# Performance work log

Hardware: AMD Instinct MI355X
Metric: run time of the kernel (lower is better)

Reference implementation:

```python
import jax, jax.numpy as jnp
import numpy as np

B, S, D, H, E, FF = 8, 512, 768, 12, 8, 3072
HD = D // H

def layernorm(x, g, b, eps=1e-5):
    mu = jnp.mean(x, axis=-1, keepdims=True)
    var = jnp.mean((x - mu) ** 2, axis=-1, keepdims=True)
    return (x - mu) * jax.lax.rsqrt(var + eps) * g + b

def setup_inputs() -> dict:
    key = jax.random.key(0)
    ks = jax.random.split(key, 16)
    sd = lambda n: 1.0 / np.sqrt(n)
    return {
        "x": jax.random.normal(ks[0], (B, S, D), jnp.float32),
        "indexes_list": jax.random.randint(ks[1], (1,), 0, E),
        "ln1_g": jnp.ones((D,), jnp.float32),
        "ln1_b": jnp.zeros((D,), jnp.float32),
        "qkv_w": jax.random.normal(ks[2], (D, 3 * D), jnp.float32) * sd(D),
        "proj_w": jax.random.normal(ks[3], (D, D), jnp.float32) * sd(D),
        "proj_b": jnp.zeros((D,), jnp.float32),
        "ln2_g": jnp.ones((D,), jnp.float32),
        "ln2_b": jnp.zeros((D,), jnp.float32),
        "switch_w": jax.random.normal(ks[4], (D, E), jnp.float32) * sd(D),
        "switch_b": jnp.zeros((E,), jnp.float32),
        "w1": jax.random.normal(ks[5], (E, D, FF), jnp.float32) * sd(D),
        "b1": jnp.zeros((E, FF), jnp.float32),
        "w2": jax.random.normal(ks[6], (E, FF, D), jnp.float32) * sd(FF),
        "b2": jnp.zeros((E, D), jnp.float32),
    }

def reference(x, indexes_list, ln1_g, ln1_b, qkv_w, proj_w, proj_b,
              ln2_g, ln2_b, switch_w, switch_b, w1, b1, w2, b2):
    # --- attention sublayer ---
    h = layernorm(x, ln1_g, ln1_b)
    qkv = (h @ qkv_w).reshape(B, S, 3, H, HD).transpose(2, 0, 3, 1, 4)  # [3,B,H,S,hd]
    q, k, v = qkv[0], qkv[1], qkv[2]
    scale = HD ** -0.5
    attn = jax.nn.softmax(jnp.einsum('bhqd,bhkd->bhqk', q, k) * scale, axis=-1)
    o = jnp.einsum('bhqk,bhkd->bhqd', attn, v).transpose(0, 2, 1, 3).reshape(B, S, D)
    x = x + o @ proj_w + proj_b
    # --- switch MoE sublayer (routes arg ignored, as in original) ---
    h = layernorm(x, ln2_g, ln2_b).reshape(B * S, D)  # [T,D]
    logits = h @ switch_w + switch_b
    routes = jnp.argmax(jax.nn.softmax(logits, axis=-1), axis=-1)  # [T]
    # dense per-expert compute, then select by route (same math as gather/scatter)
    y = jax.nn.gelu(jnp.einsum('td,edf->etf', h, w1) + b1[:, None, :], approximate=False)
    y = jax.nn.gelu(jnp.einsum('etf,efd->etd', y, w2) + b2[:, None, :], approximate=False)
    moe_out = y[routes, jnp.arange(B * S)]  # [T,D]
    return x + moe_out.reshape(B, S, D)
```

## Files before the change

kernel.cpp:

```cpp
#include <hip/hip_runtime.h>
#include <math.h>

#define T_TOK   4096
#define D_MODEL 768
#define H_HEADS 12
#define HDIM    64
#define S_SEQ   512
#define B_BATCH 8
#define E_EXP   8
#define FF_DIM  3072
#define MAX_TILES 40
#define MPAD_MAX  (MAX_TILES * 128)
#define KSPLIT  4

typedef __attribute__((ext_vector_type(8))) short short8;
typedef __attribute__((ext_vector_type(4))) float floatx4;

__device__ __forceinline__ float gelu_exact(float x) {
    return 0.5f * x * (1.0f + erff(x * 0.7071067811865476f));
}

__device__ __forceinline__ unsigned short f2bf(float f) {
    unsigned int u = __float_as_uint(f);
    u += 0x7fffu + ((u >> 16) & 1u);
    return (unsigned short)(u >> 16);
}
__device__ __forceinline__ float bf2f(unsigned short h) {
    return __uint_as_float(((unsigned int)h) << 16);
}
__device__ __forceinline__ void split_bf(float v, unsigned short& hi, unsigned short& lo) {
    hi = f2bf(v);
    lo = f2bf(v - bf2f(hi));
}

__device__ __forceinline__ void gload16(const void* g, void* l) {
    __builtin_amdgcn_global_load_lds(
        (const __attribute__((address_space(1))) unsigned int*)g,
        (__attribute__((address_space(3))) unsigned int*)l, 16, 0, 0);
}
__device__ __forceinline__ int swz3(int r) { return (r ^ (r >> 2)) & 3; }

__global__ void __launch_bounds__(256) ln_f32(const float* __restrict__ x,
                                              const float* __restrict__ g,
                                              const float* __restrict__ b,
                                              float* __restrict__ out) {
    int row = blockIdx.x;
    const float* xr = x + (size_t)row * D_MODEL;
    int tid = threadIdx.x;
    float v0 = xr[tid], v1 = xr[tid + 256], v2 = xr[tid + 512];
    float s = v0 + v1 + v2;
    float q = v0 * v0 + v1 * v1 + v2 * v2;
    for (int off = 32; off; off >>= 1) {
        s += __shfl_down(s, off);
        q += __shfl_down(q, off);
    }
    __shared__ float rs[4], rq[4], stats[2];
    int wid = tid >> 6, lane = tid & 63;
    if (lane == 0) { rs[wid] = s; rq[wid] = q; }
    __syncthreads();
    if (tid == 0) {
        float ts = rs[0] + rs[1] + rs[2] + rs[3];
        float tq = rq[0] + rq[1] + rq[2] + rq[3];
        float mu = ts * (1.0f / 768.0f);
        float var = tq * (1.0f / 768.0f) - mu * mu;
        stats[0] = mu; stats[1] = rsqrtf(var + 1e-5f);
    }
    __syncthreads();
    float mu = stats[0], rstd = stats[1];
    float* orow = out + (size_t)row * D_MODEL;
    orow[tid]       = (v0 - mu) * rstd * g[tid]       + b[tid];
    orow[tid + 256] = (v1 - mu) * rstd * g[tid + 256] + b[tid + 256];
    orow[tid + 512] = (v2 - mu) * rstd * g[tid + 512] + b[tid + 512];
}

__global__ void __launch_bounds__(256) ln_split(const float* __restrict__ x,
                                                const float* __restrict__ g,
                                                const float* __restrict__ b,
                                                unsigned short* __restrict__ ohi,
                                                unsigned short* __restrict__ olo) {
    int row = blockIdx.x;
    const float* xr = x + (size_t)row * D_MODEL;
    int tid = threadIdx.x;
    float v0 = xr[tid], v1 = xr[tid + 256], v2 = xr[tid + 512];
    float s = v0 + v1 + v2;
    float q = v0 * v0 + v1 * v1 + v2 * v2;
    for (int off = 32; off; off >>= 1) {
        s += __shfl_down(s, off);
        q += __shfl_down(q, off);
    }
    __shared__ float rs[4], rq[4], stats[2];
    int wid = tid >> 6, lane = tid & 63;
    if (lane == 0) { rs[wid] = s; rq[wid] = q; }
    __syncthreads();
    if (tid == 0) {
        float ts = rs[0] + rs[1] + rs[2] + rs[3];
        float tq = rq[0] + rq[1] + rq[2] + rq[3];
        float mu = ts * (1.0f / 768.0f);
        float var = tq * (1.0f / 768.0f) - mu * mu;
        stats[0] = mu; stats[1] = rsqrtf(var + 1e-5f);
    }
    __syncthreads();
    float mu = stats[0], rstd = stats[1];
    unsigned short* hr = ohi + (size_t)row * D_MODEL;
    unsigned short* lr = olo + (size_t)row * D_MODEL;
    float r0 = (v0 - mu) * rstd * g[tid]       + b[tid];
    float r1 = (v1 - mu) * rstd * g[tid + 256] + b[tid + 256];
    float r2 = (v2 - mu) * rstd * g[tid + 512] + b[tid + 512];
    unsigned short hi, lo;
    split_bf(r0, hi, lo); hr[tid] = hi;       lr[tid] = lo;
    split_bf(r1, hi, lo); hr[tid + 256] = hi; lr[tid + 256] = lo;
    split_bf(r2, hi, lo); hr[tid + 512] = hi; lr[tid + 512] = lo;
}

__global__ void __launch_bounds__(256) transpose_bf16(const float* __restrict__ in,
                                                      unsigned short* __restrict__ out,
                                                      int R, int C) {
    __shared__ float t[32][33];
    const float* inb = in + (size_t)blockIdx.z * R * C;
    unsigned short* outb = out + (size_t)blockIdx.z * R * C;
    int c0 = blockIdx.x * 32, r0 = blockIdx.y * 32;
    int tx = threadIdx.x & 31, ty = threadIdx.x >> 5;
#pragma unroll
    for (int rr = 0; rr < 32; rr += 8)
        t[ty + rr][tx] = inb[(size_t)(r0 + ty + rr) * C + c0 + tx];
    __syncthreads();
#pragma unroll
    for (int rr = 0; rr < 32; rr += 8)
        outb[(size_t)(c0 + ty + rr) * R + r0 + tx] = f2bf(t[tx][ty + rr]);
}

__global__ void __launch_bounds__(256) transpose_split(const float* __restrict__ in,
                                                       unsigned short* __restrict__ out_hi,
                                                       unsigned short* __restrict__ out_lo,
                                                       int R, int C) {
    __shared__ float t[32][33];
    int c0 = blockIdx.x * 32, r0 = blockIdx.y * 32;
    int tx = threadIdx.x & 31, ty = threadIdx.x >> 5;
#pragma unroll
    for (int rr = 0; rr < 32; rr += 8)
        t[ty + rr][tx] = in[(size_t)(r0 + ty + rr) * C + c0 + tx];
    __syncthreads();
#pragma unroll
    for (int rr = 0; rr < 32; rr += 8) {
        float v = t[tx][ty + rr];
        unsigned short hi, lo;
        split_bf(v, hi, lo);
        size_t idx = (size_t)(c0 + ty + rr) * R + r0 + tx;
        out_hi[idx] = hi;
        out_lo[idx] = lo;
    }
}

__global__ void __launch_bounds__(256) attn_mfma(const float* __restrict__ qkv,
                                                 unsigned short* __restrict__ ohi,
                                                 unsigned short* __restrict__ olo) {
    __shared__ __align__(16) short Kh[64][72], Kl[64][72];
    __shared__ __align__(16) short Vh[64][72], Vl[64][72];

    int qt = blockIdx.x, hh = blockIdx.y, bb = blockIdx.z;
    int tid = threadIdx.x;
    int lane = tid & 63, wv = tid >> 6;
    int lm = lane & 15, q8 = (lane >> 4) * 8, q4 = (lane >> 4) * 4;
    const size_t rstride = 3 * D_MODEL;
    const float* base = qkv + (size_t)bb * S_SEQ * rstride + hh * HDIM;

    short8 qh[2], ql[2];
    {
        const float* qrow = base + (size_t)(qt * 64 + 16 * wv + lm) * rstride;
#pragma unroll
        for (int ks = 0; ks < 2; ks++) {
            float4 v0 = *(const float4*)(qrow + ks * 32 + q8);
            float4 v1 = *(const float4*)(qrow + ks * 32 + q8 + 4);
            unsigned short h_, l_;
            short8 sh, sl;
            split_bf(v0.x * 0.125f, h_, l_); sh[0] = (short)h_; sl[0] = (short)l_;
            split_bf(v0.y * 0.125f, h_, l_); sh[1] = (short)h_; sl[1] = (short)l_;
            split_bf(v0.z * 0.125f, h_, l_); sh[2] = (short)h_; sl[2] = (short)l_;
            split_bf(v0.w * 0.125f, h_, l_); sh[3] = (short)h_; sl[3] = (short)l_;
            split_bf(v1.x * 0.125f, h_, l_); sh[4] = (short)h_; sl[4] = (short)l_;
            split_bf(v1.y * 0.125f, h_, l_); sh[5] = (short)h_; sl[5] = (short)l_;
            split_bf(v1.z * 0.125f, h_, l_); sh[6] = (short)h_; sl[6] = (short)l_;
            split_bf(v1.w * 0.125f, h_, l_); sh[7] = (short)h_; sl[7] = (short)l_;
            qh[ks] = sh; ql[ks] = sl;
        }
    }

    float m_run[4], l_run[4];
    floatx4 o_acc[4];
#pragma unroll
    for (int i = 0; i < 4; i++) {
        m_run[i] = -1e30f; l_run[i] = 0.f;
        o_acc[i] = (floatx4){0.f, 0.f, 0.f, 0.f};
    }

    int sr = tid >> 2;
    int sc0 = (tid & 3) * 16;

    for (int kt = 0; kt < 8; kt++) {
        __syncthreads();
        {
            const float* krow = base + (size_t)(kt * 64 + sr) * rstride + D_MODEL;
            const float* vrow = krow + D_MODEL;
#pragma unroll
            for (int c = 0; c < 16; c += 4) {
                float4 kv = *(const float4*)(krow + sc0 + c);
                ushort4 h4, l4; unsigned short h_, l_;
                split_bf(kv.x, h_, l_); h4.x = h_; l4.x = l_;
                split_bf(kv.y, h_, l_); h4.y = h_; l4.y = l_;
                split_bf(kv.z, h_, l_); h4.z = h_; l4.z = l_;
                split_bf(kv.w, h_, l_); h4.w = h_; l4.w = l_;
                *(ushort4*)&Kh[sr][sc0 + c] = h4;
                *(ushort4*)&Kl[sr][sc0 + c] = l4;
                float4 vv = *(const float4*)(vrow + sc0 + c);
                split_bf(vv.x, h_, l_); Vh[sc0 + c + 0][sr] = (short)h_; Vl[sc0 + c + 0][sr] = (short)l_;
                split_bf(vv.y, h_, l_); Vh[sc0 + c + 1][sr] = (short)h_; Vl[sc0 + c + 1][sr] = (short)l_;
                split_bf(vv.z, h_, l_); Vh[sc0 + c + 2][sr] = (short)h_; Vl[sc0 + c + 2][sr] = (short)l_;
                split_bf(vv.w, h_, l_); Vh[sc0 + c + 3][sr] = (short)h_; Vl[sc0 + c + 3][sr] = (short)l_;
            }
        }
        __syncthreads();

        floatx4 s_acc[4];
#pragma unroll
        for (int nt = 0; nt < 4; nt++) s_acc[nt] = (floatx4){0.f, 0.f, 0.f, 0.f};
#pragma unroll
        for (int ks = 0; ks < 2; ks++) {
#pragma unroll
            for (int nt = 0; nt < 4; nt++) {
                short8 bh = *(const short8*)&Kh[nt * 16 + lm][ks * 32 + q8];
                short8 bl = *(const short8*)&Kl[nt * 16 + lm][ks * 32 + q8];
                s_acc[nt] = __builtin_amdgcn_mfma_f32_16x16x32_bf16(qh[ks], bh, s_acc[nt], 0, 0, 0);
                s_acc[nt] = __builtin_amdgcn_mfma_f32_16x16x32_bf16(qh[ks], bl, s_acc[nt], 0, 0, 0);
                s_acc[nt] = __builtin_amdgcn_mfma_f32_16x16x32_bf16(ql[ks], bh, s_acc[nt], 0, 0, 0);
            }
        }

        float alpha_r[4];
#pragma unroll
        for (int reg = 0; reg < 4; reg++) {
            float tm = fmaxf(fmaxf(s_acc[0][reg], s_acc[1][reg]),
                             fmaxf(s_acc[2][reg], s_acc[3][reg]));
            tm = fmaxf(tm, __shfl_xor(tm, 1));
            tm = fmaxf(tm, __shfl_xor(tm, 2));
            tm = fmaxf(tm, __shfl_xor(tm, 4));
            tm = fmaxf(tm, __shfl_xor(tm, 8));
            float mn = fmaxf(m_run[reg], tm);
            alpha_r[reg] = __expf(m_run[reg] - mn);
            m_run[reg] = mn;
            float ts = 0.f;
#pragma unroll
            for (int nt = 0; nt < 4; nt++) {
                float pv = __expf(s_acc[nt][reg] - mn);
                s_acc[nt][reg] = pv;
                ts += pv;
            }
            ts += __shfl_xor(ts, 1);
            ts += __shfl_xor(ts, 2);
            ts += __shfl_xor(ts, 4);
            ts += __shfl_xor(ts, 8);
            l_run[reg] = l_run[reg] * alpha_r[reg] + ts;
        }

        __syncthreads();

#pragma unroll
        for (int nt = 0; nt < 4; nt++)
#pragma unroll
            for (int reg = 0; reg < 4; reg++) {
                unsigned short h_, l_;
                split_bf(s_acc[nt][reg], h_, l_);
                Kh[16 * wv + q4 + reg][nt * 16 + lm] = (short)h_;
                Kl[16 * wv + q4 + reg][nt * 16 + lm] = (short)l_;
            }
#pragma unroll
        for (int nt = 0; nt < 4; nt++)
#pragma unroll
            for (int reg = 0; reg < 4; reg++) o_acc[nt][reg] *= alpha_r[reg];

        __syncthreads();

#pragma unroll
        for (int ks = 0; ks < 2; ks++) {
            short8 ph = *(const short8*)&Kh[16 * wv + lm][ks * 32 + q8];
            short8 pl = *(const short8*)&Kl[16 * wv + lm][ks * 32 + q8];
#pragma unroll
            for (int nt = 0; nt < 4; nt++) {
                short8 vh = *(const short8*)&Vh[nt * 16 + lm][ks * 32 + q8];
                short8 vl = *(const short8*)&Vl[nt * 16 + lm][ks * 32 + q8];
                o_acc[nt] = __builtin_amdgcn_mfma_f32_16x16x32_bf16(ph, vh, o_acc[nt], 0, 0, 0);
                o_acc[nt] = __builtin_amdgcn_mfma_f32_16x16x32_bf16(ph, vl, o_acc[nt], 0, 0, 0);
                o_acc[nt] = __builtin_amdgcn_mfma_f32_16x16x32_bf16(pl, vh, o_acc[nt], 0, 0, 0);
            }
        }
    }

    size_t ob = (size_t)(bb * S_SEQ + qt * 64) * D_MODEL + hh * HDIM;
#pragma unroll
    for (int reg = 0; reg < 4; reg++) {
        float inv = 1.0f / l_run[reg];
#pragma unroll
        for (int nt = 0; nt < 4; nt++) {
            unsigned short h_, l_;
            split_bf(o_acc[nt][reg] * inv, h_, l_);
            size_t idx = ob + (size_t)(16 * wv + q4 + reg) * D_MODEL + nt * 16 + lm;
            ohi[idx] = h_;
            olo[idx] = l_;
        }
    }
}

__global__ void __launch_bounds__(64) router_kernel(const float* __restrict__ h2,
                                                    const float* __restrict__ sw,
                                                    const float* __restrict__ sb,
                                                    int* __restrict__ routes,
                                                    int* __restrict__ counts) {
    int t = blockIdx.x;
    int lane = threadIdx.x;
    const float* hr = h2 + (size_t)t * D_MODEL;
    float acc[8] = {};
    for (int d = lane; d < D_MODEL; d += 64) {
        float hv = hr[d];
        const float* wr = sw + (size_t)d * 8;
#pragma unroll
        for (int e = 0; e < 8; e++) acc[e] += hv * wr[e];
    }
#pragma unroll
    for (int e = 0; e < 8; e++)
        for (int off = 32; off; off >>= 1) acc[e] += __shfl_down(acc[e], off);
    if (lane == 0) {
        int best = 0;
        float bv = acc[0] + sb[0];
#pragma unroll
        for (int e = 1; e < 8; e++) {
            float v = acc[e] + sb[e];
            if (v > bv) { bv = v; best = e; }
        }
        routes[t] = best;
        atomicAdd(&counts[best], 1);
    }
}

__global__ void __launch_bounds__(256) init_kernel(int* counts, int* cursor, int* perm) {
    int idx = blockIdx.x * 256 + threadIdx.x;
    if (idx < MPAD_MAX) perm[idx] = -1;
    if (idx < 8) { counts[idx] = 0; cursor[idx] = 0; }
}

__global__ void __launch_bounds__(256) zero_tmp(float* __restrict__ t) {
    size_t i = ((size_t)blockIdx.x * 256 + threadIdx.x) * 4;
    if (i < (size_t)MPAD_MAX * D_MODEL)
        *(float4*)(t + i) = (float4){0.f, 0.f, 0.f, 0.f};
}

__global__ void moe_plan(const int* __restrict__ counts, int* pad_base,
                         int* tile_e, int* tile_row0, int* ntiles) {
    if (threadIdx.x == 0 && blockIdx.x == 0) {
        int base = 0, nt = 0;
        for (int e = 0; e < E_EXP; e++) {
            pad_base[e] = base;
            int c = counts[e];
            int nte = (c + 127) >> 7;
            for (int j = 0; j < nte; j++) {
                tile_e[nt] = e;
                tile_row0[nt] = base + j * 128;
                nt++;
            }
            base += nte * 128;
        }
        ntiles[0] = nt;
    }
}

__global__ void __launch_bounds__(256) scatter_kernel(const int* __restrict__ routes,
                                                      const int* __restrict__ pad_base,
                                                      int* __restrict__ cursor,
                                                      int* __restrict__ perm) {
    int t = blockIdx.x * 256 + threadIdx.x;
    if (t < T_TOK) {
        int e = routes[t];
        int pos = atomicAdd(&cursor[e], 1);
        perm[pad_base[e] + pos] = t;
    }
}

__global__ void __launch_bounds__(256) gather_bf16(const float* __restrict__ h2,
                                                   const int* __restrict__ perm,
                                                   unsigned short* __restrict__ Ag) {
    int g = blockIdx.x;
    int row = perm[g];
    unsigned short* dst = Ag + (size_t)g * D_MODEL;
    if (row >= 0) {
        const float* src = h2 + (size_t)row * D_MODEL;
        for (int d = threadIdx.x; d < D_MODEL; d += 256) dst[d] = f2bf(src[d]);
    } else {
        for (int d = threadIdx.x; d < D_MODEL; d += 256) dst[d] = 0;
    }
}

template <int MODE>
__global__ void __launch_bounds__(256) sgemm(const unsigned short* __restrict__ Ah_,
                                             const unsigned short* __restrict__ Al_,
                                             const unsigned short* __restrict__ Bh_,
                                             const unsigned short* __restrict__ Bl_,
                                             const float* __restrict__ bias,
                                             const float* __restrict__ resid,
                                             float* __restrict__ Cf,
                                             int N, int K) {
    __shared__ __align__(16) short Ah[2][128][32];
    __shared__ __align__(16) short Al[2][128][32];
    __shared__ __align__(16) short Bh[2][128][32];
    __shared__ __align__(16) short Bl[2][128][32];

    int row0 = blockIdx.y * 128, n0 = blockIdx.x * 128;
    int tid = threadIdx.x;
    int lane = tid & 63, wid = tid >> 6;
    int wr0 = (wid >> 1) * 64, wc0 = (wid & 1) * 64;
    int lm = lane & 15, q8 = (lane >> 4) * 8;

    int rch = lane >> 2, sl = lane & 3;
    int rst = wid * 32 + rch;
    int gsb = (sl ^ swz3(rst)) << 4;

    const unsigned short* Ahb = Ah_ + (size_t)row0 * K;
    const unsigned short* Alb = Al_ + (size_t)row0 * K;
    const unsigned short* Bhb = Bh_ + (size_t)n0 * K;
    const unsigned short* Blb = Bl_ + (size_t)n0 * K;

    const char* gAh = (const char*)(Ahb + (size_t)rst * K) + gsb;
    const char* gAl = (const char*)(Alb + (size_t)rst * K) + gsb;
    const char* gBh = (const char*)(Bhb + (size_t)rst * K) + gsb;
    const char* gBl = (const char*)(Blb + (size_t)rst * K) + gsb;
    size_t r16 = (size_t)16 * K * 2;

    auto stage = [&](int b, int t) {
        size_t kb = (size_t)t * 64;
        gload16(gAh + kb,       &Ah[b][wid * 32][0]);
        gload16(gAh + r16 + kb, &Ah[b][wid * 32 + 16][0]);
        gload16(gAl + kb,       &Al[b][wid * 32][0]);
        gload16(gAl + r16 + kb, &Al[b][wid * 32 + 16][0]);
        gload16(gBh + kb,       &Bh[b][wid * 32][0]);
        gload16(gBh + r16 + kb, &Bh[b][wid * 32 + 16][0]);
        gload16(gBl + kb,       &Bl[b][wid * 32][0]);
        gload16(gBl + r16 + kb, &Bl[b][wid * 32 + 16][0]);
    };

    floatx4 acc[4][4];
#pragma unroll
    for (int i = 0; i < 4; i++)
#pragma unroll
        for (int j = 0; j < 4; j++) acc[i][j] = (floatx4){0.f, 0.f, 0.f, 0.f};

    const int NSTEP = K >> 5;
    stage(0, 0);
    __syncthreads();

    int cur = 0;
    for (int t = 0; t < NSTEP; t++) {
        if (t + 1 < NSTEP) stage(cur ^ 1, t + 1);

        short8 ah[4], al[4], bh[4], bl[4];
#pragma unroll
        for (int i = 0; i < 4; i++) {
            int r = wr0 + i * 16 + lm;
            int bo = (q8 * 2) ^ (swz3(r) << 4);
            ah[i] = *(const short8*)((const char*)&Ah[cur][r][0] + bo);
            al[i] = *(const short8*)((const char*)&Al[cur][r][0] + bo);
        }
#pragma unroll
        for (int j = 0; j < 4; j++) {
            int r = wc0 + j * 16 + lm;
            int bo = (q8 * 2) ^ (swz3(r) << 4);
            bh[j] = *(const short8*)((const char*)&Bh[cur][r][0] + bo);
            bl[j] = *(const short8*)((const char*)&Bl[cur][r][0] + bo);
        }
#pragma unroll
        for (int i = 0; i < 4; i++)
#pragma unroll
            for (int j = 0; j < 4; j++) {
                acc[i][j] = __builtin_amdgcn_mfma_f32_16x16x32_bf16(ah[i], bh[j], acc[i][j], 0, 0, 0);
                acc[i][j] = __builtin_amdgcn_mfma_f32_16x16x32_bf16(ah[i], bl[j], acc[i][j], 0, 0, 0);
                acc[i][j] = __builtin_amdgcn_mfma_f32_16x16x32_bf16(al[i], bh[j], acc[i][j], 0, 0, 0);
            }
        __syncthreads();
        cur ^= 1;
    }

    int q4 = (lane >> 4) * 4;
#pragma unroll
    for (int i = 0; i < 4; i++) {
#pragma unroll
        for (int j = 0; j < 4; j++) {
            int c = n0 + wc0 + j * 16 + lm;
#pragma unroll
            for (int reg = 0; reg < 4; reg++) {
                int rloc = wr0 + i * 16 + q4 + reg;
                size_t idx = (size_t)(row0 + rloc) * N + c;
                float v = acc[i][j][reg];
                if constexpr (MODE == 0) Cf[idx] = v;
                else                     Cf[idx] = resid[idx] + v + bias[c];
            }
        }
    }
}

template <int MODE>
__global__ void __launch_bounds__(256) mgemm(const unsigned short* __restrict__ A,
                                             const unsigned short* __restrict__ Bt,
                                             const float* __restrict__ bias,
                                             const float* __restrict__ resid,
                                             float* __restrict__ Cf,
                                             unsigned short* __restrict__ Cb,
                                             int N, int K,
                                             const int* __restrict__ perm,
                                             const int* __restrict__ tile_e,
                                             const int* __restrict__ tile_row0,
                                             const int* __restrict__ ntiles) {
    __shared__ __align__(16) short As[2][128][64];
    __shared__ __align__(16) short Bs[2][128][64];

    if ((int)blockIdx.y >= ntiles[0]) return;
    int e = tile_e[blockIdx.y];
    int row0 = tile_row0[blockIdx.y];
    Bt += (size_t)e * N * K;
    bias += (size_t)e * N;
    int n0 = blockIdx.x * 128;

    int tid = threadIdx.x;
    int lane = tid & 63, wid = tid >> 6;
    int wr0 = (wid >> 1) * 64, wc0 = (wid & 1) * 64;
    int lm = lane & 15, q8 = (lane >> 4) * 8;

    int rl = lane >> 3, sl = lane & 7;
    int gsb = (sl ^ rl) << 4;

    const unsigned short* Abase = A + (size_t)row0 * K;
    const unsigned short* Bbase = Bt + (size_t)n0 * K;
    const char* gA = (const char*)(Abase + (size_t)(wid * 32 + rl) * K) + gsb;
    const char* gB = (const char*)(Bbase + (size_t)(wid * 32 + rl) * K) + gsb;

    auto stage = [&](int b, int t) {
        size_t kb = (size_t)t * 128;
#pragma unroll
        for (int c = 0; c < 4; c++) {
            gload16(gA + (size_t)c * 16 * K + kb, &As[b][wid * 32 + c * 8][0]);
            gload16(gB + (size_t)c * 16 * K + kb, &Bs[b][wid * 32 + c * 8][0]);
        }
    };

    floatx4 acc[4][4];
#pragma unroll
    for (int i = 0; i < 4; i++)
#pragma unroll
        for (int j = 0; j < 4; j++) acc[i][j] = (floatx4){0.f, 0.f, 0.f, 0.f};

    const int NSTEP = K >> 6;
    stage(0, 0);
    __syncthreads();

    int cur = 0;
    for (int t = 0; t < NSTEP; t++) {
        if (t + 1 < NSTEP) stage(cur ^ 1, t + 1);

#pragma unroll
        for (int ks = 0; ks < 2; ks++) {
            short8 af[4], bfr[4];
#pragma unroll
            for (int i = 0; i < 4; i++) {
                int r = wr0 + i * 16 + lm;
                int bo = (ks * 64 + q8 * 2) ^ ((r & 7) << 4);
                af[i] = *(const short8*)((const char*)&As[cur][r][0] + bo);
            }
#pragma unroll
            for (int j = 0; j < 4; j++) {
                int r = wc0 + j * 16 + lm;
                int bo = (ks * 64 + q8 * 2) ^ ((r & 7) << 4);
                bfr[j] = *(const short8*)((const char*)&Bs[cur][r][0] + bo);
            }
#pragma unroll
            for (int i = 0; i < 4; i++)
#pragma unroll
                for (int j = 0; j < 4; j++)
                    acc[i][j] = __builtin_amdgcn_mfma_f32_16x16x32_bf16(af[i], bfr[j], acc[i][j], 0, 0, 0);
        }
        __syncthreads();
        cur ^= 1;
    }

    int q4 = (lane >> 4) * 4;
#pragma unroll
    for (int i = 0; i < 4; i++) {
#pragma unroll
        for (int j = 0; j < 4; j++) {
            int c = n0 + wc0 + j * 16 + lm;
#pragma unroll
            for (int reg = 0; reg < 4; reg++) {
                int rloc = wr0 + i * 16 + q4 + reg;
                float v = acc[i][j][reg];
                if constexpr (MODE == 2) {
                    Cb[(size_t)(row0 + rloc) * N + c] = f2bf(gelu_exact(v + bias[c]));
                } else {
                    int t = perm[row0 + rloc];
                    if (t >= 0) {
                        size_t idx = (size_t)t * N + c;
                        Cf[idx] = resid[idx] + gelu_exact(v + bias[c]);
                    }
                }
            }
        }
    }
}

__global__ void __launch_bounds__(256) kgemm(const unsigned short* __restrict__ A,
                                             const unsigned short* __restrict__ Bt,
                                             float* __restrict__ tmp,
                                             int N, int K,
                                             const int* __restrict__ tile_e,
                                             const int* __restrict__ tile_row0,
                                             const int* __restrict__ ntiles) {
    __shared__ __align__(16) short As[2][128][64];
    __shared__ __align__(16) short Bs[2][128][64];

    if ((int)blockIdx.y >= ntiles[0]) return;
    int e = tile_e[blockIdx.y];
    int row0 = tile_row0[blockIdx.y];
    Bt += (size_t)e * N * K;
    int n0 = blockIdx.x * 128;
    const int KLEN = K / KSPLIT;
    size_t kbase = (size_t)blockIdx.z * KLEN * 2;

    int tid = threadIdx.x;
    int lane = tid & 63, wid = tid >> 6;
    int wr0 = (wid >> 1) * 64, wc0 = (wid & 1) * 64;
    int lm = lane & 15, q8 = (lane >> 4) * 8;

    int rl = lane >> 3, sl = lane & 7;
    int gsb = (sl ^ rl) << 4;

    const unsigned short* Abase = A + (size_t)row0 * K;
    const unsigned short* Bbase = Bt + (size_t)n0 * K;
    const char* gA = (const char*)(Abase + (size_t)(wid * 32 + rl) * K) + gsb + kbase;
    const char* gB = (const char*)(Bbase + (size_t)(wid * 32 + rl) * K) + gsb + kbase;

    auto stage = [&](int b, int t) {
        size_t kb = (size_t)t * 128;
#pragma unroll
        for (int c = 0; c < 4; c++) {
            gload16(gA + (size_t)c * 16 * K + kb, &As[b][wid * 32 + c * 8][0]);
            gload16(gB + (size_t)c * 16 * K + kb, &Bs[b][wid * 32 + c * 8][0]);
        }
    };

    floatx4 acc[4][4];
#pragma unroll
    for (int i = 0; i < 4; i++)
#pragma unroll
        for (int j = 0; j < 4; j++) acc[i][j] = (floatx4){0.f, 0.f, 0.f, 0.f};

    const int NSTEP = KLEN >> 6;
    stage(0, 0);
    __syncthreads();

    int cur = 0;
    for (int t = 0; t < NSTEP; t++) {
        if (t + 1 < NSTEP) stage(cur ^ 1, t + 1);

#pragma unroll
        for (int ks = 0; ks < 2; ks++) {
            short8 af[4], bfr[4];
#pragma unroll
            for (int i = 0; i < 4; i++) {
                int r = wr0 + i * 16 + lm;
                int bo = (ks * 64 + q8 * 2) ^ ((r & 7) << 4);
                af[i] = *(const short8*)((const char*)&As[cur][r][0] + bo);
            }
#pragma unroll
            for (int j = 0; j < 4; j++) {
                int r = wc0 + j * 16 + lm;
                int bo = (ks * 64 + q8 * 2) ^ ((r & 7) << 4);
                bfr[j] = *(const short8*)((const char*)&Bs[cur][r][0] + bo);
            }
#pragma unroll
            for (int i = 0; i < 4; i++)
#pragma unroll
                for (int j = 0; j < 4; j++)
                    acc[i][j] = __builtin_amdgcn_mfma_f32_16x16x32_bf16(af[i], bfr[j], acc[i][j], 0, 0, 0);
        }
        __syncthreads();
        cur ^= 1;
    }

    int q4 = (lane >> 4) * 4;
#pragma unroll
    for (int i = 0; i < 4; i++) {
#pragma unroll
        for (int j = 0; j < 4; j++) {
            int c = n0 + wc0 + j * 16 + lm;
#pragma unroll
            for (int reg = 0; reg < 4; reg++) {
                int rloc = wr0 + i * 16 + q4 + reg;
                atomicAdd(&tmp[(size_t)(row0 + rloc) * N + c], acc[i][j][reg]);
            }
        }
    }
}

__global__ void __launch_bounds__(256) moe_epilogue(const float* __restrict__ tmp,
                                                    const int* __restrict__ perm,
                                                    const int* __restrict__ routes,
                                                    const float* __restrict__ b2,
                                                    const float* __restrict__ x1,
                                                    float* __restrict__ out) {
    int g = blockIdx.x;
    int t = perm[g];
    if (t < 0) return;
    int e = routes[t];
    const float* tr = tmp + (size_t)g * D_MODEL;
    const float* br = b2 + (size_t)e * D_MODEL;
    const float* xr = x1 + (size_t)t * D_MODEL;
    float* orow = out + (size_t)t * D_MODEL;
    int d = threadIdx.x;
    orow[d]       = xr[d]       + gelu_exact(tr[d]       + br[d]);
    orow[d + 256] = xr[d + 256] + gelu_exact(tr[d + 256] + br[d + 256]);
    orow[d + 512] = xr[d + 512] + gelu_exact(tr[d + 512] + br[d + 512]);
}

extern "C" void kernel_launch(void* const* d_in, const int* in_sizes, int n_in,
                              void* d_out, int out_size, void* d_ws, size_t ws_size,
                              hipStream_t stream) {
    const float* x      = (const float*)d_in[0];
    const float* ln1_g  = (const float*)d_in[2];
    const float* ln1_b  = (const float*)d_in[3];
    const float* qkv_w  = (const float*)d_in[4];
    const float* proj_w = (const float*)d_in[5];
    const float* proj_b = (const float*)d_in[6];
    const float* ln2_g  = (const float*)d_in[7];
    const float* ln2_b  = (const float*)d_in[8];
    const float* sw     = (const float*)d_in[9];
    const float* sb     = (const float*)d_in[10];
    const float* w1     = (const float*)d_in[11];
    const float* b1     = (const float*)d_in[12];
    const float* w2     = (const float*)d_in[13];
    const float* b2     = (const float*)d_in[14];
    float* out = (float*)d_out;

    char* p = (char*)d_ws;
    float*          qkv = (float*)p;
    float*          h   = (float*)p;
    unsigned short* y1  = (unsigned short*)p;
    p += (size_t)T_TOK * 2304 * 4;
    unsigned short* h_hi = (unsigned short*)p; p += (size_t)T_TOK * D_MODEL * 2;
    unsigned short* h_lo = (unsigned short*)p; p += (size_t)T_TOK * D_MODEL * 2;
    unsigned short* o_hi = h_hi;
    unsigned short* o_lo = h_lo;
    float* x1 = (float*)p; p += (size_t)T_TOK * D_MODEL * 4;
    unsigned short* Ag     = (unsigned short*)p;
    unsigned short* qwt_hi = (unsigned short*)p;
    unsigned short* qwt_lo = qwt_hi + (size_t)2304 * 768;
    p += (size_t)MPAD_MAX * D_MODEL * 2;
    unsigned short* pwt_hi = (unsigned short*)p; p += (size_t)768 * 768 * 2;
    unsigned short* pwt_lo = (unsigned short*)p; p += (size_t)768 * 768 * 2;
    unsigned short* w1t = (unsigned short*)p; p += (size_t)E_EXP * 3072 * 768 * 2;
    unsigned short* w2t = (unsigned short*)p; p += (size_t)E_EXP * 768 * 3072 * 2;
    int* routes    = (int*)p;
    int* perm      = routes + T_TOK;
    int* counts    = perm + MPAD_MAX;
    int* cursor    = counts + 8;
    int* pad_base  = cursor + 8;
    int* tile_e    = pad_base + 8;
    int* tile_row0 = tile_e + MAX_TILES;
    int* ntiles    = tile_row0 + MAX_TILES;
    char* pa = (char*)(ntiles + 1);
    pa = (char*)(((size_t)pa + 15) & ~(size_t)15);
    float* tmp = (float*)pa;

    transpose_split<<<dim3(2304 / 32, 768 / 32), 256, 0, stream>>>(qkv_w, qwt_hi, qwt_lo, 768, 2304);
    transpose_split<<<dim3(768 / 32, 768 / 32), 256, 0, stream>>>(proj_w, pwt_hi, pwt_lo, 768, 768);
    transpose_bf16<<<dim3(3072 / 32, 768 / 32, 8), 256, 0, stream>>>(w1, w1t, 768, 3072);
    transpose_bf16<<<dim3(768 / 32, 3072 / 32, 8), 256, 0, stream>>>(w2, w2t, 3072, 768);

    ln_split<<<T_TOK, 256, 0, stream>>>(x, ln1_g, ln1_b, h_hi, h_lo);
    sgemm<0><<<dim3(2304 / 128, T_TOK / 128), 256, 0, stream>>>(
        h_hi, h_lo, qwt_hi, qwt_lo, nullptr, nullptr, qkv, 2304, 768);
    attn_mfma<<<dim3(S_SEQ / 64, H_HEADS, B_BATCH), 256, 0, stream>>>(qkv, o_hi, o_lo);
    sgemm<1><<<dim3(768 / 128, T_TOK / 128), 256, 0, stream>>>(
        o_hi, o_lo, pwt_hi, pwt_lo, proj_b, x, x1, 768, 768);
    ln_f32<<<T_TOK, 256, 0, stream>>>(x1, ln2_g, ln2_b, h);
    init_kernel<<<(MPAD_MAX + 255) / 256, 256, 0, stream>>>(counts, cursor, perm);
    zero_tmp<<<(MPAD_MAX * D_MODEL / 4 + 255) / 256, 256, 0, stream>>>(tmp);
    router_kernel<<<T_TOK, 64, 0, stream>>>(h, sw, sb, routes, counts);
    moe_plan<<<1, 1, 0, stream>>>(counts, pad_base, tile_e, tile_row0, ntiles);
    scatter_kernel<<<T_TOK / 256, 256, 0, stream>>>(routes, pad_base, cursor, perm);
    gather_bf16<<<MPAD_MAX, 256, 0, stream>>>(h, perm, Ag);
    mgemm<2><<<dim3(FF_DIM / 128, MAX_TILES), 256, 0, stream>>>(
        Ag, w1t, b1, nullptr, nullptr, y1, FF_DIM, 768,
        perm, tile_e, tile_row0, ntiles);
    kgemm<<<dim3(D_MODEL / 128, MAX_TILES, KSPLIT), 256, 0, stream>>>(
        y1, w2t, tmp, D_MODEL, 3072, tile_e, tile_row0, ntiles);
    moe_epilogue<<<MPAD_MAX, 256, 0, stream>>>(tmp, perm, routes, b2, x1, out);
}
```

Before: 672.8 us.

## Replace split-K atomic second MoE GEMM with narrow-tile direct GEMM and fused epilogue

The second expert GEMM drops its 4-way split-K with atomic float adds into a zeroed temp buffer. It now runs each output tile over the full K with a narrower 64-column N tile to keep enough blocks in flight. Bias, GELU and the residual add are fused into the GEMM epilogue and written straight to the scattered output rows. This removes the zero_tmp and moe_epilogue launches along with the atomic traffic, at the cost of a longer serial K loop per block and fewer, smaller blocks.

```diff
diff --git a/kernel.cpp b/kernel.cpp
--- a/kernel.cpp
+++ b/kernel.cpp
@@ -11,7 +11,6 @@
 #define FF_DIM  3072
 #define MAX_TILES 40
 #define MPAD_MAX  (MAX_TILES * 128)
-#define KSPLIT  4
 
 typedef __attribute__((ext_vector_type(8))) short short8;
 typedef __attribute__((ext_vector_type(4))) float floatx4;
@@ -346,12 +345,6 @@
     if (idx < 8) { counts[idx] = 0; cursor[idx] = 0; }
 }
 
-__global__ void __launch_bounds__(256) zero_tmp(float* __restrict__ t) {
-    size_t i = ((size_t)blockIdx.x * 256 + threadIdx.x) * 4;
-    if (i < (size_t)MPAD_MAX * D_MODEL)
-        *(float4*)(t + i) = (float4){0.f, 0.f, 0.f, 0.f};
-}
-
 __global__ void moe_plan(const int* __restrict__ counts, int* pad_base,
                          int* tile_e, int* tile_row0, int* ntiles) {
     if (threadIdx.x == 0 && blockIdx.x == 0) {
@@ -610,27 +603,29 @@
     }
 }
 
-__global__ void __launch_bounds__(256) kgemm(const unsigned short* __restrict__ A,
+__global__ void __launch_bounds__(256) dgemm(const unsigned short* __restrict__ A,
                                              const unsigned short* __restrict__ Bt,
-                                             float* __restrict__ tmp,
+                                             const float* __restrict__ bias,
+                                             const float* __restrict__ resid,
+                                             float* __restrict__ Cf,
                                              int N, int K,
+                                             const int* __restrict__ perm,
                                              const int* __restrict__ tile_e,
                                              const int* __restrict__ tile_row0,
                                              const int* __restrict__ ntiles) {
     __shared__ __align__(16) short As[2][128][64];
-    __shared__ __align__(16) short Bs[2][128][64];
+    __shared__ __align__(16) short Bs[2][64][64];
 
     if ((int)blockIdx.y >= ntiles[0]) return;
     int e = tile_e[blockIdx.y];
     int row0 = tile_row0[blockIdx.y];
     Bt += (size_t)e * N * K;
-    int n0 = blockIdx.x * 128;
-    const int KLEN = K / KSPLIT;
-    size_t kbase = (size_t)blockIdx.z * KLEN * 2;
+    bias += (size_t)e * N;
+    int n0 = blockIdx.x * 64;
 
     int tid = threadIdx.x;
     int lane = tid & 63, wid = tid >> 6;
-    int wr0 = (wid >> 1) * 64, wc0 = (wid & 1) * 64;
+    int wr0 = (wid >> 1) * 64, wc0 = (wid & 1) * 32;
     int lm = lane & 15, q8 = (lane >> 4) * 8;
 
     int rl = lane >> 3, sl = lane & 7;
@@ -638,25 +633,26 @@
 
     const unsigned short* Abase = A + (size_t)row0 * K;
     const unsigned short* Bbase = Bt + (size_t)n0 * K;
-    const char* gA = (const char*)(Abase + (size_t)(wid * 32 + rl) * K) + gsb + kbase;
-    const char* gB = (const char*)(Bbase + (size_t)(wid * 32 + rl) * K) + gsb + kbase;
+    const char* gA = (const char*)(Abase + (size_t)(wid * 32 + rl) * K) + gsb;
+    const char* gB = (const char*)(Bbase + (size_t)(wid * 16 + rl) * K) + gsb;
 
     auto stage = [&](int b, int t) {
         size_t kb = (size_t)t * 128;
 #pragma unroll
-        for (int c = 0; c < 4; c++) {
+        for (int c = 0; c < 4; c++)
             gload16(gA + (size_t)c * 16 * K + kb, &As[b][wid * 32 + c * 8][0]);
-            gload16(gB + (size_t)c * 16 * K + kb, &Bs[b][wid * 32 + c * 8][0]);
-        }
+#pragma unroll
+        for (int c = 0; c < 2; c++)
+            gload16(gB + (size_t)c * 16 * K + kb, &Bs[b][wid * 16 + c * 8][0]);
     };
 
-    floatx4 acc[4][4];
+    floatx4 acc[4][2];
 #pragma unroll
     for (int i = 0; i < 4; i++)
 #pragma unroll
-        for (int j = 0; j < 4; j++) acc[i][j] = (floatx4){0.f, 0.f, 0.f, 0.f};
-
-    const int NSTEP = KLEN >> 6;
+        for (int j = 0; j < 2; j++) acc[i][j] = (floatx4){0.f, 0.f, 0.f, 0.f};
+
+    const int NSTEP = K >> 6;
     stage(0, 0);
     __syncthreads();
 
@@ -666,7 +662,7 @@
 
 #pragma unroll
         for (int ks = 0; ks < 2; ks++) {
-            short8 af[4], bfr[4];
+            short8 af[4], bfr[2];
 #pragma unroll
             for (int i = 0; i < 4; i++) {
                 int r = wr0 + i * 16 + lm;
@@ -674,7 +670,7 @@
                 af[i] = *(const short8*)((const char*)&As[cur][r][0] + bo);
             }
 #pragma unroll
-            for (int j = 0; j < 4; j++) {
+            for (int j = 0; j < 2; j++) {
                 int r = wc0 + j * 16 + lm;
                 int bo = (ks * 64 + q8 * 2) ^ ((r & 7) << 4);
                 bfr[j] = *(const short8*)((const char*)&Bs[cur][r][0] + bo);
@@ -682,7 +678,7 @@
 #pragma unroll
             for (int i = 0; i < 4; i++)
 #pragma unroll
-                for (int j = 0; j < 4; j++)
+                for (int j = 0; j < 2; j++)
                     acc[i][j] = __builtin_amdgcn_mfma_f32_16x16x32_bf16(af[i], bfr[j], acc[i][j], 0, 0, 0);
         }
         __syncthreads();
@@ -693,35 +689,19 @@
 #pragma unroll
     for (int i = 0; i < 4; i++) {
 #pragma unroll
-        for (int j = 0; j < 4; j++) {
+        for (int j = 0; j < 2; j++) {
             int c = n0 + wc0 + j * 16 + lm;
 #pragma unroll
             for (int reg = 0; reg < 4; reg++) {
                 int rloc = wr0 + i * 16 + q4 + reg;
-                atomicAdd(&tmp[(size_t)(row0 + rloc) * N + c], acc[i][j][reg]);
-            }
-        }
-    }
-}
-
-__global__ void __launch_bounds__(256) moe_epilogue(const float* __restrict__ tmp,
-                                                    const int* __restrict__ perm,
-                                                    const int* __restrict__ routes,
-                                                    const float* __restrict__ b2,
-                                                    const float* __restrict__ x1,
-                                                    float* __restrict__ out) {
-    int g = blockIdx.x;
-    int t = perm[g];
-    if (t < 0) return;
-    int e = routes[t];
-    const float* tr = tmp + (size_t)g * D_MODEL;
-    const float* br = b2 + (size_t)e * D_MODEL;
-    const float* xr = x1 + (size_t)t * D_MODEL;
-    float* orow = out + (size_t)t * D_MODEL;
-    int d = threadIdx.x;
-    orow[d]       = xr[d]       + gelu_exact(tr[d]       + br[d]);
-    orow[d + 256] = xr[d + 256] + gelu_exact(tr[d + 256] + br[d + 256]);
-    orow[d + 512] = xr[d + 512] + gelu_exact(tr[d + 512] + br[d + 512]);
+                int t = perm[row0 + rloc];
+                if (t >= 0) {
+                    size_t idx = (size_t)t * N + c;
+                    Cf[idx] = resid[idx] + gelu_exact(acc[i][j][reg] + bias[c]);
+                }
+            }
+        }
+    }
 }
 
 extern "C" void kernel_launch(void* const* d_in, const int* in_sizes, int n_in,
@@ -769,9 +749,6 @@
     int* tile_e    = pad_base + 8;
     int* tile_row0 = tile_e + MAX_TILES;
     int* ntiles    = tile_row0 + MAX_TILES;
-    char* pa = (char*)(ntiles + 1);
-    pa = (char*)(((size_t)pa + 15) & ~(size_t)15);
-    float* tmp = (float*)pa;
 
     transpose_split<<<dim3(2304 / 32, 768 / 32), 256, 0, stream>>>(qkv_w, qwt_hi, qwt_lo, 768, 2304);
     transpose_split<<<dim3(768 / 32, 768 / 32), 256, 0, stream>>>(proj_w, pwt_hi, pwt_lo, 768, 768);
@@ -786,7 +763,6 @@
         o_hi, o_lo, pwt_hi, pwt_lo, proj_b, x, x1, 768, 768);
     ln_f32<<<T_TOK, 256, 0, stream>>>(x1, ln2_g, ln2_b, h);
     init_kernel<<<(MPAD_MAX + 255) / 256, 256, 0, stream>>>(counts, cursor, perm);
-    zero_tmp<<<(MPAD_MAX * D_MODEL / 4 + 255) / 256, 256, 0, stream>>>(tmp);
     router_kernel<<<T_TOK, 64, 0, stream>>>(h, sw, sb, routes, counts);
     moe_plan<<<1, 1, 0, stream>>>(counts, pad_base, tile_e, tile_row0, ntiles);
     scatter_kernel<<<T_TOK / 256, 256, 0, stream>>>(routes, pad_base, cursor, perm);
@@ -794,7 +770,7 @@
     mgemm<2><<<dim3(FF_DIM / 128, MAX_TILES), 256, 0, stream>>>(
         Ag, w1t, b1, nullptr, nullptr, y1, FF_DIM, 768,
         perm, tile_e, tile_row0, ntiles);
-    kgemm<<<dim3(D_MODEL / 128, MAX_TILES, KSPLIT), 256, 0, stream>>>(
-        y1, w2t, tmp, D_MODEL, 3072, tile_e, tile_row0, ntiles);
-    moe_epilogue<<<MPAD_MAX, 256, 0, stream>>>(tmp, perm, routes, b2, x1, out);
-}
+    dgemm<<<dim3(D_MODEL / 64, MAX_TILES), 256, 0, stream>>>(
+        y1, w2t, b2, x1, out, D_MODEL, 3072,
+        perm, tile_e, tile_row0, ntiles);
+}
```

Result: faster. 598.3 us (-11.1%).
